# Optimization experiments

Measured on AMD Instinct MI355X. Metric: run time of the kernel, lower is better.

The kernel has to match this reference:

```python
import jax, jax.numpy as jnp
import numpy as np

S = 72
IMG_W, IMG_H = 640, 360
STRIDE = 32
FMAP_H, FMAP_W = IMG_H // STRIDE, IMG_W // STRIDE  # 11, 20
N_OFFSETS = S
N_STRIPS = S - 1
ANGLES = np.array([15.0, 22.0, 30.0, 39.0, 49.0, 60.0, 72.0, 80.0, 90.0, 100.0, 108.0, 120.0, 131.0, 141.0, 150.0, 158.0, 165.0])
N_ANG = 17
N_PRED = 2 + 2 + 1 + N_OFFSETS  # 77
N_EDGE = FMAP_W + 2 * FMAP_H    # 42
N_PROP = N_ANG * N_EDGE         # 714
NMS_THRES = 15.0
BACKBONE_C = 512
CONV_C = 1024


def _make_anchors():
    anchor_ys = np.linspace(1.0, 0.0, N_OFFSETS)
    tan = np.tan(np.deg2rad(ANGLES))
    def side(origins):
        out = np.zeros((N_ANG, N_PRED, len(origins)), np.float32)
        for i, (sx, sy) in enumerate(origins):
            out[:, 2, i] = 1.0 - sy
            out[:, 3, i] = sx
            out[:, 5:, i] = (sx + (sy - anchor_ys)[None, :] / tan[:, None]) * IMG_W
        return out.reshape(N_ANG * N_PRED, len(origins))
    left = side([(0.0, y) for y in np.linspace(1.0, 0.0, FMAP_H)])
    right = side([(1.0, y) for y in np.linspace(1.0, 0.0, FMAP_H)])
    bottom = side([(x, 1.0) for x in np.linspace(1.0, 0.0, FMAP_W)])
    anchors = np.zeros((N_ANG * N_PRED, FMAP_H, FMAP_W), np.float32)
    anchors[:, :, 0] = left
    anchors[:, :, -1] = right
    anchors[:, -1, :] = bottom
    edge = np.concatenate([anchors[:, :, 0], anchors[:, :, -1], anchors[:, -1, :]], 1)  # [1309,42]
    anch_dim = edge.reshape(N_ANG, N_PRED, N_EDGE).transpose(2, 0, 1).reshape(N_PROP, N_PRED)
    return jnp.asarray(anchors), jnp.asarray(anch_dim)


def setup_inputs():
    key = jax.random.key(0)
    ks = jax.random.split(key, 4)
    B = 32
    feat = jax.random.normal(ks[0], (B, BACKBONE_C, FMAP_H, FMAP_W), jnp.float32)
    W_conv = jax.random.normal(ks[1], (CONV_C, BACKBONE_C), jnp.float32) * 0.02
    b_conv = jnp.zeros((CONV_C,), jnp.float32)
    W_cls = jax.random.normal(ks[2], (2 * N_ANG, CONV_C), jnp.float32) * 0.02
    b_cls = jnp.zeros((2 * N_ANG,), jnp.float32)
    W_reg = jax.random.normal(ks[3], (N_ANG * (N_OFFSETS + 1), CONV_C), jnp.float32) * 0.02
    b_reg = jnp.zeros((N_ANG * (N_OFFSETS + 1),), jnp.float32)
    anchors, anchors_anchor_dim = _make_anchors()
    return {"feat": feat, "W_conv": W_conv, "b_conv": b_conv, "W_cls": W_cls, "b_cls": b_cls,
            "W_reg": W_reg, "b_reg": b_reg, "anchors": anchors, "anchors_anchor_dim": anchors_anchor_dim}


def _proposals(feat, W_conv, b_conv, W_cls, b_cls, W_reg, b_reg, anchors):
    B = feat.shape[0]
    features = jnp.einsum('bchw,oc->bohw', feat, W_conv) + b_conv[None, :, None, None]
    cls_f = jnp.einsum('bchw,oc->bohw', features, W_cls) + b_cls[None, :, None, None]
    reg_f = jnp.einsum('bchw,oc->bohw', features, W_reg) + b_reg[None, :, None, None]
    anch = anchors.reshape(N_ANG, N_PRED, FMAP_H, FMAP_W)
    cls_r = cls_f.reshape(B, N_ANG, 2, FMAP_H, FMAP_W)
    reg_r = reg_f.reshape(B, N_ANG, N_OFFSETS + 1, FMAP_H, FMAP_W)
    # slots 0:2 <- cls logits (set), slots 2:4 <- anchor (copied), slots 4: <- anchor + reg
    mid = jnp.broadcast_to(anch[None, :, 2:4], (B, N_ANG, 2, FMAP_H, FMAP_W))
    tail = anch[None, :, 4:] + reg_r
    lane = jnp.concatenate([cls_r, mid, tail], axis=2)  # [B,17,77,h,w]
    # gather the three feature-map edges: left col, right col, bottom row
    edges = jnp.concatenate([lane[:, :, :, :, 0], lane[:, :, :, :, -1], lane[:, :, :, -1, :]], axis=3)  # [B,17,77,42]
    return edges.transpose(0, 3, 1, 2).reshape(B, N_PROP, N_PRED)  # [B,714,77]


def _nms_one(props, scores):
    # greedy line-NMS over proposals of one image, shapes static
    order = jnp.argsort(-scores)
    p = props[order]
    start = jnp.clip(jnp.round(p[:, 2] * N_STRIPS), 0.0, float(N_STRIPS))
    end = jnp.clip(start + p[:, 4] - 1.0, 0.0, float(N_STRIPS))
    xs = p[:, 5:]  # [N,72]
    s = jnp.maximum(start[:, None], start[None, :])
    e = jnp.minimum(end[:, None], end[None, :])
    idx = jnp.arange(N_OFFSETS, dtype=p.dtype)
    m = (idx[None, None, :] >= s[..., None]) & (idx[None, None, :] <= e[..., None])  # [N,N,72]
    diff = jnp.abs(xs[:, None, :] - xs[None, :, :])  # [N,N,72]
    cnt = e - s + 1.0
    dist = jnp.where(cnt > 0, jnp.sum(diff * m, -1) / jnp.maximum(cnt, 1.0), jnp.inf)
    sup = dist < NMS_THRES
    n = p.shape[0]
    pos = jnp.arange(n)
    def step(suppressed, i):
        keep_i = ~suppressed[i]
        suppressed = suppressed | (keep_i & sup[i] & (pos > i))
        return suppressed, keep_i
    _, keep_sorted = jax.lax.scan(step, jnp.zeros(n, bool), pos)
    return jnp.zeros(n, bool).at[order].set(keep_sorted)


def reference(feat, W_conv, b_conv, W_cls, b_cls, W_reg, b_reg, anchors, anchors_anchor_dim):
    proposals = _proposals(feat, W_conv, b_conv, W_cls, b_cls, W_reg, b_reg, anchors)
    scores = jax.nn.softmax(proposals[..., :2], axis=-1)[..., 1]  # [B,714]
    keep_mask = jax.lax.map(lambda pr: _nms_one(pr[0], pr[1]), (proposals, scores))  # [B,714]
    return proposals, keep_mask, scores
```

## Files before the change

### kernel.cpp

```cpp
#include <hip/hip_runtime.h>
#include <math.h>

#define NB     32
#define FH     11
#define FW     20
#define CIN    512
#define CMID   1024
#define NANG   17
#define NPREDD 77
#define NEDGE  42
#define NPROPP 714
#define NOFF   72
#define NCLS   34
#define NREGR  1241
#define N2PAD  1280
#define MTOT   1344
#define NSTRIPSF 71.0f
#define PADK   40

typedef unsigned long long u64;
typedef unsigned short ushortt;
typedef short s8v __attribute__((ext_vector_type(8)));
typedef float f4v __attribute__((ext_vector_type(4)));

__device__ inline ushortt f2bf(float f) {
    unsigned u = __float_as_uint(f);
    u += 0x7fffu + ((u >> 16) & 1u);
    return (ushortt)(u >> 16);
}
__device__ inline float bf2f(ushortt h) {
    return __uint_as_float(((unsigned)h) << 16);
}

__global__ __launch_bounds__(256) void k_gather_split(const float* __restrict__ feat,
                                                      ushortt* __restrict__ Ahi,
                                                      ushortt* __restrict__ Alo)
{
    int idx = blockIdx.x * 256 + threadIdx.x;
    int m = idx >> 9, c = idx & 511;
    int b = m / NEDGE, e = m - b * NEDGE;
    int h, w;
    if (e < FH)          { h = e;      w = 0;      }
    else if (e < 2 * FH) { h = e - FH; w = FW - 1; }
    else                 { h = FH - 1; w = e - 2 * FH; }
    float v = feat[((size_t)(b * CIN + c) * FH + h) * FW + w];
    ushortt hi = f2bf(v);
    Ahi[idx] = hi;
    Alo[idx] = f2bf(v - bf2f(hi));
}

__global__ __launch_bounds__(256) void k_gemm1m(const ushortt* __restrict__ Ahi,
                                                const ushortt* __restrict__ Alo,
                                                const float* __restrict__ W,
                                                const float* __restrict__ bias,
                                                ushortt* __restrict__ Chi,
                                                ushortt* __restrict__ Clo)
{
    const int K = CIN, N = CMID;
    __shared__ __align__(16) ushortt Ash[64 * PADK], Asl[64 * PADK];
    __shared__ __align__(16) ushortt Bsh[64 * PADK], Bsl[64 * PADK];
    int tid = threadIdx.x;
    int m0 = blockIdx.y * 64, n0 = blockIdx.x * 64;
    int srow = tid >> 2, sg = tid & 3;
    int lane = tid & 63, wv = tid >> 6;
    int wm = (wv & 1) * 32, wn = (wv >> 1) * 32;
    int quad = lane >> 4, l15 = lane & 15;

    f4v acc[2][2];
#pragma unroll
    for (int i = 0; i < 2; ++i)
#pragma unroll
        for (int j = 0; j < 2; ++j) acc[i][j] = (f4v){0.f, 0.f, 0.f, 0.f};

    const ushortt* Ahp = Ahi + (size_t)(m0 + srow) * K + sg * 8;
    const ushortt* Alp = Alo + (size_t)(m0 + srow) * K + sg * 8;
    const float*   Wp  = W   + (size_t)(n0 + srow) * K + sg * 8;

    for (int k0 = 0; k0 < K; k0 += 32) {
        __syncthreads();
        s8v av = *(const s8v*)(Ahp + k0);
        s8v lv = *(const s8v*)(Alp + k0);
        float4 w0 = *(const float4*)(Wp + k0);
        float4 w1 = *(const float4*)(Wp + k0 + 4);
        float wf[8] = {w0.x, w0.y, w0.z, w0.w, w1.x, w1.y, w1.z, w1.w};
        s8v wh, wl;
#pragma unroll
        for (int j = 0; j < 8; ++j) {
            ushortt h = f2bf(wf[j]);
            wh[j] = (short)h;
            wl[j] = (short)f2bf(wf[j] - bf2f(h));
        }
        *(s8v*)&Ash[srow * PADK + sg * 8] = av;
        *(s8v*)&Asl[srow * PADK + sg * 8] = lv;
        *(s8v*)&Bsh[srow * PADK + sg * 8] = wh;
        *(s8v*)&Bsl[srow * PADK + sg * 8] = wl;
        __syncthreads();
        s8v ah[2], al[2], bh[2], bl[2];
#pragma unroll
        for (int s = 0; s < 2; ++s) {
            ah[s] = *(const s8v*)&Ash[(wm + s * 16 + l15) * PADK + quad * 8];
            al[s] = *(const s8v*)&Asl[(wm + s * 16 + l15) * PADK + quad * 8];
            bh[s] = *(const s8v*)&Bsh[(wn + s * 16 + l15) * PADK + quad * 8];
            bl[s] = *(const s8v*)&Bsl[(wn + s * 16 + l15) * PADK + quad * 8];
        }
#pragma unroll
        for (int sm = 0; sm < 2; ++sm)
#pragma unroll
            for (int sn = 0; sn < 2; ++sn) {
                acc[sm][sn] = __builtin_amdgcn_mfma_f32_16x16x32_bf16(al[sm], bl[sn], acc[sm][sn], 0, 0, 0);
                acc[sm][sn] = __builtin_amdgcn_mfma_f32_16x16x32_bf16(al[sm], bh[sn], acc[sm][sn], 0, 0, 0);
                acc[sm][sn] = __builtin_amdgcn_mfma_f32_16x16x32_bf16(ah[sm], bl[sn], acc[sm][sn], 0, 0, 0);
                acc[sm][sn] = __builtin_amdgcn_mfma_f32_16x16x32_bf16(ah[sm], bh[sn], acc[sm][sn], 0, 0, 0);
            }
    }
#pragma unroll
    for (int sm = 0; sm < 2; ++sm)
#pragma unroll
        for (int sn = 0; sn < 2; ++sn)
#pragma unroll
            for (int r = 0; r < 4; ++r) {
                int m = m0 + wm + sm * 16 + quad * 4 + r;
                int n = n0 + wn + sn * 16 + l15;
                float v = acc[sm][sn][r] + bias[n];
                ushortt h = f2bf(v);
                Chi[(size_t)m * N + n] = h;
                Clo[(size_t)m * N + n] = f2bf(v - bf2f(h));
            }
}

__global__ __launch_bounds__(256) void k_gemm2m(const ushortt* __restrict__ Ahi,
                                                const ushortt* __restrict__ Alo,
                                                const float* __restrict__ Wcls,
                                                const float* __restrict__ bcls,
                                                const float* __restrict__ Wreg,
                                                const float* __restrict__ breg,
                                                float* __restrict__ C)
{
    const int K = CMID;
    __shared__ __align__(16) ushortt Ash[64 * PADK], Asl[64 * PADK];
    __shared__ __align__(16) ushortt Bsh[64 * PADK], Bsl[64 * PADK];
    int tid = threadIdx.x;
    int m0 = blockIdx.y * 64, n0 = blockIdx.x * 64;
    int srow = tid >> 2, sg = tid & 3;
    int lane = tid & 63, wv = tid >> 6;
    int wm = (wv & 1) * 32, wn = (wv >> 1) * 32;
    int quad = lane >> 4, l15 = lane & 15;

    f4v acc[2][2];
#pragma unroll
    for (int i = 0; i < 2; ++i)
#pragma unroll
        for (int j = 0; j < 2; ++j) acc[i][j] = (f4v){0.f, 0.f, 0.f, 0.f};

    const ushortt* Ahp = Ahi + (size_t)(m0 + srow) * K + sg * 8;
    const ushortt* Alp = Alo + (size_t)(m0 + srow) * K + sg * 8;
    int nrow = n0 + srow;
    const float* Wp = Wcls;
    bool wvalid = true;
    if (nrow < NCLS)              Wp = Wcls + (size_t)nrow * K + sg * 8;
    else if (nrow < NCLS + NREGR) Wp = Wreg + (size_t)(nrow - NCLS) * K + sg * 8;
    else                          wvalid = false;

    for (int k0 = 0; k0 < K; k0 += 32) {
        __syncthreads();
        s8v av = *(const s8v*)(Ahp + k0);
        s8v lv = *(const s8v*)(Alp + k0);
        float4 w0, w1;
        if (wvalid) {
            w0 = *(const float4*)(Wp + k0);
            w1 = *(const float4*)(Wp + k0 + 4);
        } else {
            w0 = make_float4(0.f, 0.f, 0.f, 0.f);
            w1 = w0;
        }
        float wf[8] = {w0.x, w0.y, w0.z, w0.w, w1.x, w1.y, w1.z, w1.w};
        s8v wh, wl;
#pragma unroll
        for (int j = 0; j < 8; ++j) {
            ushortt h = f2bf(wf[j]);
            wh[j] = (short)h;
            wl[j] = (short)f2bf(wf[j] - bf2f(h));
        }
        *(s8v*)&Ash[srow * PADK + sg * 8] = av;
        *(s8v*)&Asl[srow * PADK + sg * 8] = lv;
        *(s8v*)&Bsh[srow * PADK + sg * 8] = wh;
        *(s8v*)&Bsl[srow * PADK + sg * 8] = wl;
        __syncthreads();
        s8v ah[2], al[2], bh[2], bl[2];
#pragma unroll
        for (int s = 0; s < 2; ++s) {
            ah[s] = *(const s8v*)&Ash[(wm + s * 16 + l15) * PADK + quad * 8];
            al[s] = *(const s8v*)&Asl[(wm + s * 16 + l15) * PADK + quad * 8];
            bh[s] = *(const s8v*)&Bsh[(wn + s * 16 + l15) * PADK + quad * 8];
            bl[s] = *(const s8v*)&Bsl[(wn + s * 16 + l15) * PADK + quad * 8];
        }
#pragma unroll
        for (int sm = 0; sm < 2; ++sm)
#pragma unroll
            for (int sn = 0; sn < 2; ++sn) {
                acc[sm][sn] = __builtin_amdgcn_mfma_f32_16x16x32_bf16(al[sm], bl[sn], acc[sm][sn], 0, 0, 0);
                acc[sm][sn] = __builtin_amdgcn_mfma_f32_16x16x32_bf16(al[sm], bh[sn], acc[sm][sn], 0, 0, 0);
                acc[sm][sn] = __builtin_amdgcn_mfma_f32_16x16x32_bf16(ah[sm], bl[sn], acc[sm][sn], 0, 0, 0);
                acc[sm][sn] = __builtin_amdgcn_mfma_f32_16x16x32_bf16(ah[sm], bh[sn], acc[sm][sn], 0, 0, 0);
            }
    }
#pragma unroll
    for (int sm = 0; sm < 2; ++sm)
#pragma unroll
        for (int sn = 0; sn < 2; ++sn)
#pragma unroll
            for (int r = 0; r < 4; ++r) {
                int m = m0 + wm + sm * 16 + quad * 4 + r;
                int n = n0 + wn + sn * 16 + l15;
                float bb = (n < NCLS) ? bcls[n] : ((n < NCLS + NREGR) ? breg[n - NCLS] : 0.f);
                C[(size_t)m * N2PAD + n] = acc[sm][sn][r] + bb;
            }
}

__global__ __launch_bounds__(256) void k_assemble(const float* __restrict__ C2,
                                                  const float* __restrict__ AD,
                                                  float* __restrict__ outP,
                                                  float* __restrict__ outS,
                                                  float* __restrict__ startv,
                                                  float* __restrict__ endv,
                                                  float* __restrict__ xsel)
{
    int mb = blockIdx.x;
    int b = mb / NEDGE, e = mb - b * NEDGE;
    const float* c2 = C2 + (size_t)mb * N2PAD;
    int tid = threadIdx.x;
    for (int idx = tid; idx < NANG * NPREDD; idx += 256) {
        int a = idx / NPREDD, p = idx - a * NPREDD;
        int prop = e * NANG + a;
        float v;
        if (p < 2) v = c2[a * 2 + p];
        else {
            v = AD[prop * NPREDD + p];
            if (p >= 4) v += c2[NCLS + a * 73 + (p - 4)];
        }
        outP[((size_t)b * NPROPP + prop) * NPREDD + p] = v;
    }
    if (tid < NANG) {
        int a = tid, prop = e * NANG + a;
        float c0 = c2[2 * a], c1 = c2[2 * a + 1];
        float mx = fmaxf(c0, c1);
        float e0 = expf(c0 - mx), e1 = expf(c1 - mx);
        outS[b * NPROPP + prop] = e1 / (e0 + e1);
        float p2 = AD[prop * NPREDD + 2];
        float p4 = AD[prop * NPREDD + 4] + c2[NCLS + a * 73];
        float st = fminf(fmaxf(rintf(p2 * NSTRIPSF), 0.0f), NSTRIPSF);
        float en = fminf(fmaxf(st + p4 - 1.0f, 0.0f), NSTRIPSF);
        startv[b * 720 + prop] = st;
        endv[b * 720 + prop] = en;
        int ksi = (int)st;
        xsel[b * 720 + prop] = AD[prop * NPREDD + 5 + ksi] + c2[NCLS + a * 73 + ksi + 1];
    }
}

__global__ __launch_bounds__(128) void k_sort(const float* __restrict__ scores,
                                              int* __restrict__ order)
{
    int b = blockIdx.x, tile = blockIdx.y, tid = threadIdx.x;
    __shared__ __align__(16) float s[720];
    for (int x = tid; x < 720; x += 128)
        s[x] = (x < NPROPP) ? scores[b * NPROPP + x] : -1e30f;
    __syncthreads();
    int i = tile * 128 + tid;
    if (i >= NPROPP) return;
    float si = s[i];
    int r = 0;
#pragma unroll 4
    for (int j4 = 0; j4 < 720; j4 += 4) {
        float4 v = *(const float4*)&s[j4];
        r += (v.x > si) || (v.x == si && (j4 + 0) < i);
        r += (v.y > si) || (v.y == si && (j4 + 1) < i);
        r += (v.z > si) || (v.z == si && (j4 + 2) < i);
        r += (v.w > si) || (v.w == si && (j4 + 3) < i);
    }
    order[b * 720 + r] = i;
}

__global__ __launch_bounds__(256) void k_supmat(const float* __restrict__ outP,
                                                const float* __restrict__ startv,
                                                const float* __restrict__ endv,
                                                const float* __restrict__ xsel,
                                                const int* __restrict__ order,
                                                u64* __restrict__ sup)
{
    int jt = blockIdx.x, it = blockIdx.y, b = blockIdx.z;
    int i0 = it * 64, j0 = jt * 64;
    int tid = threadIdx.x;
    if (j0 + 63 < i0) {
        if (tid < 64) {
            int il = i0 + tid;
            if (il < NPROPP) sup[((size_t)b * NPROPP + il) * 12 + jt] = 0ull;
        }
        return;
    }
    __shared__ float SI[64], EI[64], XI[64];
    __shared__ float SJ[64], EJ[64], XJ[64];
    __shared__ int   OI[64], OJ[64];
    if (tid < 128) {
        int side = tid >> 6, q = tid & 63;
        int pos = (side ? j0 : i0) + q;
        int o = (pos < NPROPP) ? order[b * 720 + pos] : -1;
        float st = (o >= 0) ? startv[b * 720 + o] : 0.f;
        float en = (o >= 0) ? endv[b * 720 + o] : -2.f;
        float xv = (o >= 0) ? xsel[b * 720 + o] : 0.f;
        if (!side) { SI[q] = st; EI[q] = en; XI[q] = xv; OI[q] = o; }
        else       { SJ[q] = st; EJ[q] = en; XJ[q] = xv; OJ[q] = o; }
    }
    __syncthreads();
    int lane = tid & 63, w = tid >> 6;
    int j = j0 + lane;
    float sj = SJ[lane], ej = EJ[lane], xj = XJ[lane];
    const float* basexs = outP + (size_t)b * NPROPP * NPREDD + 5;
#pragma unroll 1
    for (int rep = 0; rep < 16; ++rep) {
        int iloc = w * 16 + rep;
        int il = i0 + iloc;
        float si = SI[iloc], ei = EI[iloc];
        float s = fmaxf(si, sj), e = fminf(ei, ej);
        float cnt = e - s + 1.0f;
        bool sp = false;
        if (cnt > 0.f) {
            if (e < s) {
                sp = true;
            } else {
                int ks = (int)s, ke = (int)e;
                if (si == sj && ke == ks) {
                    sp = (fabsf(XI[iloc] - xj) / fmaxf(cnt, 1.0f)) < 15.0f;
                } else {
                    const float* xi  = basexs + (size_t)OI[iloc] * NPREDD;
                    const float* xjp = basexs + (size_t)OJ[lane] * NPREDD;
                    float sum = 0.f;
                    for (int k = ks; k <= ke; ++k)
                        sum += fabsf(xi[k] - xjp[k]);
                    sp = (sum / fmaxf(cnt, 1.0f)) < 15.0f;
                }
            }
        }
        bool valid = (il < NPROPP) && (j < NPROPP) && (j > il);
        u64 msk = __ballot(valid && sp);
        if (lane == 0 && il < NPROPP)
            sup[((size_t)b * NPROPP + il) * 12 + jt] = msk;
    }
}

__global__ __launch_bounds__(256) void k_scan(const u64* __restrict__ sup,
                                              const int* __restrict__ order,
                                              float* __restrict__ keep_out)
{
    int b = blockIdx.x, tid = threadIdx.x;
    int lane = tid & 63;
    __shared__ u64 K[12], NS[12];
    __shared__ int changed;
    const u64* base = sup + (size_t)b * NPROPP * 12;

    int r0 = tid, r1 = tid + 256, r2 = tid + 512;
    u64 row0[12], row1[12], row2[12];
#pragma unroll
    for (int t = 0; t < 12; ++t) {
        row0[t] = base[(size_t)r0 * 12 + t];
        row1[t] = (r1 < NPROPP) ? base[(size_t)r1 * 12 + t] : 0ull;
        row2[t] = (r2 < NPROPP) ? base[(size_t)r2 * 12 + t] : 0ull;
    }
    if (tid < 12) {
        K[tid] = (tid < 11) ? ~0ull : ((1ull << (NPROPP - 704)) - 1ull);
        NS[tid] = 0ull;
    }
    __syncthreads();

    for (int sweep = 0; sweep < 720; ++sweep) {
        u64 m0 = 0ull - ((K[r0 >> 6] >> (r0 & 63)) & 1ull);
        u64 m1 = (r1 < NPROPP) ? (0ull - ((K[r1 >> 6] >> (r1 & 63)) & 1ull)) : 0ull;
        u64 m2 = (r2 < NPROPP) ? (0ull - ((K[r2 >> 6] >> (r2 & 63)) & 1ull)) : 0ull;
        unsigned lo[12], hi[12];
#pragma unroll
        for (int t = 0; t < 12; ++t) {
            u64 a = (row0[t] & m0) | (row1[t] & m1) | (row2[t] & m2);
            lo[t] = (unsigned)a;
            hi[t] = (unsigned)(a >> 32);
        }
#pragma unroll
        for (int s = 1; s < 64; s <<= 1) {
#pragma unroll
            for (int t = 0; t < 12; ++t) {
                lo[t] |= __shfl_xor(lo[t], s, 64);
                hi[t] |= __shfl_xor(hi[t], s, 64);
            }
        }
        if (tid == 0) changed = 0;
        if (lane == 0) {
#pragma unroll
            for (int t = 0; t < 12; ++t)
                atomicOr(&NS[t], ((u64)hi[t] << 32) | (u64)lo[t]);
        }
        __syncthreads();
        if (tid < 12) {
            u64 valid = (tid < 11) ? ~0ull : ((1ull << (NPROPP - 704)) - 1ull);
            u64 nk = valid & ~NS[tid];
            if (nk != K[tid]) changed = 1;
            K[tid] = nk;
            NS[tid] = 0ull;
        }
        __syncthreads();
        if (!changed) break;
    }
    if (r0 < NPROPP)
        keep_out[b * NPROPP + order[b * 720 + r0]] =
            ((K[r0 >> 6] >> (r0 & 63)) & 1ull) ? 1.f : 0.f;
    if (r1 < NPROPP)
        keep_out[b * NPROPP + order[b * 720 + r1]] =
            ((K[r1 >> 6] >> (r1 & 63)) & 1ull) ? 1.f : 0.f;
    if (r2 < NPROPP)
        keep_out[b * NPROPP + order[b * 720 + r2]] =
            ((K[r2 >> 6] >> (r2 & 63)) & 1ull) ? 1.f : 0.f;
}

extern "C" void kernel_launch(void* const* d_in, const int* in_sizes, int n_in,
                              void* d_out, int out_size, void* d_ws, size_t ws_size,
                              hipStream_t stream)
{
    const float* feat  = (const float*)d_in[0];
    const float* Wconv = (const float*)d_in[1];
    const float* bconv = (const float*)d_in[2];
    const float* Wcls  = (const float*)d_in[3];
    const float* bcls  = (const float*)d_in[4];
    const float* Wreg  = (const float*)d_in[5];
    const float* breg  = (const float*)d_in[6];
    const float* AD    = (const float*)d_in[8];

    float* out  = (float*)d_out;
    float* outP = out;
    float* outK = out + (size_t)NB * NPROPP * NPREDD;
    float* outS = outK + (size_t)NB * NPROPP;

    float* ws = (float*)d_ws;
    ushortt* A1hi = (ushortt*)ws;
    ushortt* A1lo = (ushortt*)(ws + 344064);
    ushortt* A2hi = (ushortt*)(ws + 688128);
    ushortt* A2lo = (ushortt*)(ws + 1376256);
    float*   C2   = ws + 2064384;
    float* startv = ws;
    float* endv   = ws + 23040;
    int*   order  = (int*)(ws + 46080);
    u64*   sup    = (u64*)(ws + 69120);
    float* xsel   = ws + 617472;

    k_gather_split<<<dim3(2688),       dim3(256), 0, stream>>>(feat, A1hi, A1lo);
    k_gemm1m      <<<dim3(16, 21),     dim3(256), 0, stream>>>(A1hi, A1lo, Wconv, bconv, A2hi, A2lo);
    k_gemm2m      <<<dim3(20, 21),     dim3(256), 0, stream>>>(A2hi, A2lo, Wcls, bcls, Wreg, breg, C2);
    k_assemble    <<<dim3(MTOT),       dim3(256), 0, stream>>>(C2, AD, outP, outS, startv, endv, xsel);
    k_sort        <<<dim3(NB, 6),      dim3(128), 0, stream>>>(outS, order);
    k_supmat      <<<dim3(12, 12, NB), dim3(256), 0, stream>>>(outP, startv, endv, xsel, order, sup);
    k_scan        <<<dim3(NB),         dim3(256), 0, stream>>>(sup, order, outK);
}
```

Before: 192.4 us.

## Fuse edge gather into first GEMM and split K across two thread halves

Removes the separate gather/split kernel by having the first GEMM read edge features directly from the feature map and convert them to bf16 hi/lo in registers. Both GEMMs now launch 512 threads per block, with each 256-thread half handling one half of K; partial sums are reduced through shared memory before the epilogue. This targets the low occupancy of the small 336/420-block grids and saves one launch plus a global round trip. The cost is strided, uncoalesced feature loads in the first GEMM and extra shared memory and synchronisation for the reduction.

Result: slower. 197.3 us (+2.5%).

```diff
diff --git a/kernel.cpp b/kernel.cpp
--- a/kernel.cpp
+++ b/kernel.cpp
@@ -32,39 +32,33 @@
     return __uint_as_float(((unsigned)h) << 16);
 }
 
-__global__ __launch_bounds__(256) void k_gather_split(const float* __restrict__ feat,
-                                                      ushortt* __restrict__ Ahi,
-                                                      ushortt* __restrict__ Alo)
-{
-    int idx = blockIdx.x * 256 + threadIdx.x;
-    int m = idx >> 9, c = idx & 511;
-    int b = m / NEDGE, e = m - b * NEDGE;
+__global__ __launch_bounds__(512) void k_gemm1f(const float* __restrict__ feat,
+                                                const float* __restrict__ W,
+                                                const float* __restrict__ bias,
+                                                ushortt* __restrict__ Chi,
+                                                ushortt* __restrict__ Clo)
+{
+    const int K = CIN, K2 = CIN / 2, N = CMID;
+    __shared__ __align__(16) ushortt Ash[2][64 * PADK], Asl[2][64 * PADK];
+    __shared__ __align__(16) ushortt Bsh[2][64 * PADK], Bsl[2][64 * PADK];
+    __shared__ __align__(16) float Pr[64 * 68];
+    int tid = threadIdx.x;
+    int half = tid >> 8, t = tid & 255;
+    int m0 = blockIdx.y * 64, n0 = blockIdx.x * 64;
+    int srow = t >> 2, sg = t & 3;
+    int lane = t & 63, wv = t >> 6;
+    int wm = (wv & 1) * 32, wn = (wv >> 1) * 32;
+    int quad = lane >> 4, l15 = lane & 15;
+
+    int m = m0 + srow;
+    int bb_ = m / NEDGE, e = m - bb_ * NEDGE;
     int h, w;
     if (e < FH)          { h = e;      w = 0;      }
     else if (e < 2 * FH) { h = e - FH; w = FW - 1; }
     else                 { h = FH - 1; w = e - 2 * FH; }
-    float v = feat[((size_t)(b * CIN + c) * FH + h) * FW + w];
-    ushortt hi = f2bf(v);
-    Ahi[idx] = hi;
-    Alo[idx] = f2bf(v - bf2f(hi));
-}
-
-__global__ __launch_bounds__(256) void k_gemm1m(const ushortt* __restrict__ Ahi,
-                                                const ushortt* __restrict__ Alo,
-                                                const float* __restrict__ W,
-                                                const float* __restrict__ bias,
-                                                ushortt* __restrict__ Chi,
-                                                ushortt* __restrict__ Clo)
-{
-    const int K = CIN, N = CMID;
-    __shared__ __align__(16) ushortt Ash[64 * PADK], Asl[64 * PADK];
-    __shared__ __align__(16) ushortt Bsh[64 * PADK], Bsl[64 * PADK];
-    int tid = threadIdx.x;
-    int m0 = blockIdx.y * 64, n0 = blockIdx.x * 64;
-    int srow = tid >> 2, sg = tid & 3;
-    int lane = tid & 63, wv = tid >> 6;
-    int wm = (wv & 1) * 32, wn = (wv >> 1) * 32;
-    int quad = lane >> 4, l15 = lane & 15;
+    const float* fbase = feat + ((size_t)(bb_ * CIN) * FH + h) * FW + w;
+    const int cbase = half * K2 + sg * 8;
+    const float* Wp = W + (size_t)(n0 + srow) * K + half * K2 + sg * 8;
 
     f4v acc[2][2];
 #pragma unroll
@@ -72,36 +66,38 @@
 #pragma unroll
         for (int j = 0; j < 2; ++j) acc[i][j] = (f4v){0.f, 0.f, 0.f, 0.f};
 
-    const ushortt* Ahp = Ahi + (size_t)(m0 + srow) * K + sg * 8;
-    const ushortt* Alp = Alo + (size_t)(m0 + srow) * K + sg * 8;
-    const float*   Wp  = W   + (size_t)(n0 + srow) * K + sg * 8;
-
-    for (int k0 = 0; k0 < K; k0 += 32) {
-        __syncthreads();
-        s8v av = *(const s8v*)(Ahp + k0);
-        s8v lv = *(const s8v*)(Alp + k0);
+    for (int k0 = 0; k0 < K2; k0 += 32) {
+        __syncthreads();
+        s8v ah8, al8;
+#pragma unroll
+        for (int j = 0; j < 8; ++j) {
+            float v = fbase[(size_t)(cbase + k0 + j) * (FH * FW)];
+            ushortt hh_ = f2bf(v);
+            ah8[j] = (short)hh_;
+            al8[j] = (short)f2bf(v - bf2f(hh_));
+        }
         float4 w0 = *(const float4*)(Wp + k0);
         float4 w1 = *(const float4*)(Wp + k0 + 4);
         float wf[8] = {w0.x, w0.y, w0.z, w0.w, w1.x, w1.y, w1.z, w1.w};
         s8v wh, wl;
 #pragma unroll
         for (int j = 0; j < 8; ++j) {
-            ushortt h = f2bf(wf[j]);
-            wh[j] = (short)h;
-            wl[j] = (short)f2bf(wf[j] - bf2f(h));
-        }
-        *(s8v*)&Ash[srow * PADK + sg * 8] = av;
-        *(s8v*)&Asl[srow * PADK + sg * 8] = lv;
-        *(s8v*)&Bsh[srow * PADK + sg * 8] = wh;
-        *(s8v*)&Bsl[srow * PADK + sg * 8] = wl;
+            ushortt hh_ = f2bf(wf[j]);
+            wh[j] = (short)hh_;
+            wl[j] = (short)f2bf(wf[j] - bf2f(hh_));
+        }
+        *(s8v*)&Ash[half][srow * PADK + sg * 8] = ah8;
+        *(s8v*)&Asl[half][srow * PADK + sg * 8] = al8;
+        *(s8v*)&Bsh[half][srow * PADK + sg * 8] = wh;
+        *(s8v*)&Bsl[half][srow * PADK + sg * 8] = wl;
         __syncthreads();
         s8v ah[2], al[2], bh[2], bl[2];
 #pragma unroll
         for (int s = 0; s < 2; ++s) {
-            ah[s] = *(const s8v*)&Ash[(wm + s * 16 + l15) * PADK + quad * 8];
-            al[s] = *(const s8v*)&Asl[(wm + s * 16 + l15) * PADK + quad * 8];
-            bh[s] = *(const s8v*)&Bsh[(wn + s * 16 + l15) * PADK + quad * 8];
-            bl[s] = *(const s8v*)&Bsl[(wn + s * 16 + l15) * PADK + quad * 8];
+            ah[s] = *(const s8v*)&Ash[half][(wm + s * 16 + l15) * PADK + quad * 8];
+            al[s] = *(const s8v*)&Asl[half][(wm + s * 16 + l15) * PADK + quad * 8];
+            bh[s] = *(const s8v*)&Bsh[half][(wn + s * 16 + l15) * PADK + quad * 8];
+            bl[s] = *(const s8v*)&Bsl[half][(wn + s * 16 + l15) * PADK + quad * 8];
         }
 #pragma unroll
         for (int sm = 0; sm < 2; ++sm)
@@ -113,22 +109,35 @@
                 acc[sm][sn] = __builtin_amdgcn_mfma_f32_16x16x32_bf16(ah[sm], bh[sn], acc[sm][sn], 0, 0, 0);
             }
     }
-#pragma unroll
-    for (int sm = 0; sm < 2; ++sm)
-#pragma unroll
-        for (int sn = 0; sn < 2; ++sn)
-#pragma unroll
-            for (int r = 0; r < 4; ++r) {
-                int m = m0 + wm + sm * 16 + quad * 4 + r;
-                int n = n0 + wn + sn * 16 + l15;
-                float v = acc[sm][sn][r] + bias[n];
-                ushortt h = f2bf(v);
-                Chi[(size_t)m * N + n] = h;
-                Clo[(size_t)m * N + n] = f2bf(v - bf2f(h));
-            }
-}
-
-__global__ __launch_bounds__(256) void k_gemm2m(const ushortt* __restrict__ Ahi,
+    __syncthreads();
+    if (half == 1) {
+#pragma unroll
+        for (int sm = 0; sm < 2; ++sm)
+#pragma unroll
+            for (int sn = 0; sn < 2; ++sn)
+#pragma unroll
+                for (int r = 0; r < 4; ++r)
+                    Pr[(wm + sm * 16 + quad * 4 + r) * 68 + wn + sn * 16 + l15] = acc[sm][sn][r];
+    }
+    __syncthreads();
+    if (half == 0) {
+#pragma unroll
+        for (int sm = 0; sm < 2; ++sm)
+#pragma unroll
+            for (int sn = 0; sn < 2; ++sn)
+#pragma unroll
+                for (int r = 0; r < 4; ++r) {
+                    int mm = m0 + wm + sm * 16 + quad * 4 + r;
+                    int n = n0 + wn + sn * 16 + l15;
+                    float v = (acc[sm][sn][r] + Pr[(wm + sm * 16 + quad * 4 + r) * 68 + wn + sn * 16 + l15]) + bias[n];
+                    ushortt hh_ = f2bf(v);
+                    Chi[(size_t)mm * N + n] = hh_;
+                    Clo[(size_t)mm * N + n] = f2bf(v - bf2f(hh_));
+                }
+    }
+}
+
+__global__ __launch_bounds__(512) void k_gemm2f(const ushortt* __restrict__ Ahi,
                                                 const ushortt* __restrict__ Alo,
                                                 const float* __restrict__ Wcls,
                                                 const float* __restrict__ bcls,
@@ -136,32 +145,34 @@
                                                 const float* __restrict__ breg,
                                                 float* __restrict__ C)
 {
-    const int K = CMID;
-    __shared__ __align__(16) ushortt Ash[64 * PADK], Asl[64 * PADK];
-    __shared__ __align__(16) ushortt Bsh[64 * PADK], Bsl[64 * PADK];
+    const int K = CMID, K2 = CMID / 2;
+    __shared__ __align__(16) ushortt Ash[2][64 * PADK], Asl[2][64 * PADK];
+    __shared__ __align__(16) ushortt Bsh[2][64 * PADK], Bsl[2][64 * PADK];
+    __shared__ __align__(16) float Pr[64 * 68];
     int tid = threadIdx.x;
+    int half = tid >> 8, t = tid & 255;
     int m0 = blockIdx.y * 64, n0 = blockIdx.x * 64;
-    int srow = tid >> 2, sg = tid & 3;
-    int lane = tid & 63, wv = tid >> 6;
+    int srow = t >> 2, sg = t & 3;
+    int lane = t & 63, wv = t >> 6;
     int wm = (wv & 1) * 32, wn = (wv >> 1) * 32;
     int quad = lane >> 4, l15 = lane & 15;
 
-    f4v acc[2][2];
-#pragma unroll
-    for (int i = 0; i < 2; ++i)
-#pragma unroll
-        for (int j = 0; j < 2; ++j) acc[i][j] = (f4v){0.f, 0.f, 0.f, 0.f};
-
-    const ushortt* Ahp = Ahi + (size_t)(m0 + srow) * K + sg * 8;
-    const ushortt* Alp = Alo + (size_t)(m0 + srow) * K + sg * 8;
+    const ushortt* Ahp = Ahi + (size_t)(m0 + srow) * K + half * K2 + sg * 8;
+    const ushortt* Alp = Alo + (size_t)(m0 + srow) * K + half * K2 + sg * 8;
     int nrow = n0 + srow;
     const float* Wp = Wcls;
     bool wvalid = true;
-    if (nrow < NCLS)              Wp = Wcls + (size_t)nrow * K + sg * 8;
-    else if (nrow < NCLS + NREGR) Wp = Wreg + (size_t)(nrow - NCLS) * K + sg * 8;
+    if (nrow < NCLS)              Wp = Wcls + (size_t)nrow * K + half * K2 + sg * 8;
+    else if (nrow < NCLS + NREGR) Wp = Wreg + (size_t)(nrow - NCLS) * K + half * K2 + sg * 8;
     else                          wvalid = false;
 
-    for (int k0 = 0; k0 < K; k0 += 32) {
+    f4v acc[2][2];
+#pragma unroll
+    for (int i = 0; i < 2; ++i)
+#pragma unroll
+        for (int j = 0; j < 2; ++j) acc[i][j] = (f4v){0.f, 0.f, 0.f, 0.f};
+
+    for (int k0 = 0; k0 < K2; k0 += 32) {
         __syncthreads();
         s8v av = *(const s8v*)(Ahp + k0);
         s8v lv = *(const s8v*)(Alp + k0);
@@ -177,22 +188,22 @@
         s8v wh, wl;
 #pragma unroll
         for (int j = 0; j < 8; ++j) {
-            ushortt h = f2bf(wf[j]);
-            wh[j] = (short)h;
-            wl[j] = (short)f2bf(wf[j] - bf2f(h));
-        }
-        *(s8v*)&Ash[srow * PADK + sg * 8] = av;
-        *(s8v*)&Asl[srow * PADK + sg * 8] = lv;
-        *(s8v*)&Bsh[srow * PADK + sg * 8] = wh;
-        *(s8v*)&Bsl[srow * PADK + sg * 8] = wl;
+            ushortt hh_ = f2bf(wf[j]);
+            wh[j] = (short)hh_;
+            wl[j] = (short)f2bf(wf[j] - bf2f(hh_));
+        }
+        *(s8v*)&Ash[half][srow * PADK + sg * 8] = av;
+        *(s8v*)&Asl[half][srow * PADK + sg * 8] = lv;
+        *(s8v*)&Bsh[half][srow * PADK + sg * 8] = wh;
+        *(s8v*)&Bsl[half][srow * PADK + sg * 8] = wl;
         __syncthreads();
         s8v ah[2], al[2], bh[2], bl[2];
 #pragma unroll
         for (int s = 0; s < 2; ++s) {
-            ah[s] = *(const s8v*)&Ash[(wm + s * 16 + l15) * PADK + quad * 8];
-            al[s] = *(const s8v*)&Asl[(wm + s * 16 + l15) * PADK + quad * 8];
-            bh[s] = *(const s8v*)&Bsh[(wn + s * 16 + l15) * PADK + quad * 8];
-            bl[s] = *(const s8v*)&Bsl[(wn + s * 16 + l15) * PADK + quad * 8];
+            ah[s] = *(const s8v*)&Ash[half][(wm + s * 16 + l15) * PADK + quad * 8];
+            al[s] = *(const s8v*)&Asl[half][(wm + s * 16 + l15) * PADK + quad * 8];
+            bh[s] = *(const s8v*)&Bsh[half][(wn + s * 16 + l15) * PADK + quad * 8];
+            bl[s] = *(const s8v*)&Bsl[half][(wn + s * 16 + l15) * PADK + quad * 8];
         }
 #pragma unroll
         for (int sm = 0; sm < 2; ++sm)
@@ -204,17 +215,31 @@
                 acc[sm][sn] = __builtin_amdgcn_mfma_f32_16x16x32_bf16(ah[sm], bh[sn], acc[sm][sn], 0, 0, 0);
             }
     }
-#pragma unroll
-    for (int sm = 0; sm < 2; ++sm)
-#pragma unroll
-        for (int sn = 0; sn < 2; ++sn)
-#pragma unroll
-            for (int r = 0; r < 4; ++r) {
-                int m = m0 + wm + sm * 16 + quad * 4 + r;
-                int n = n0 + wn + sn * 16 + l15;
-                float bb = (n < NCLS) ? bcls[n] : ((n < NCLS + NREGR) ? breg[n - NCLS] : 0.f);
-                C[(size_t)m * N2PAD + n] = acc[sm][sn][r] + bb;
-            }
+    __syncthreads();
+    if (half == 1) {
+#pragma unroll
+        for (int sm = 0; sm < 2; ++sm)
+#pragma unroll
+            for (int sn = 0; sn < 2; ++sn)
+#pragma unroll
+                for (int r = 0; r < 4; ++r)
+                    Pr[(wm + sm * 16 + quad * 4 + r) * 68 + wn + sn * 16 + l15] = acc[sm][sn][r];
+    }
+    __syncthreads();
+    if (half == 0) {
+#pragma unroll
+        for (int sm = 0; sm < 2; ++sm)
+#pragma unroll
+            for (int sn = 0; sn < 2; ++sn)
+#pragma unroll
+                for (int r = 0; r < 4; ++r) {
+                    int mm = m0 + wm + sm * 16 + quad * 4 + r;
+                    int n = n0 + wn + sn * 16 + l15;
+                    float bb = (n < NCLS) ? bcls[n] : ((n < NCLS + NREGR) ? breg[n - NCLS] : 0.f);
+                    C[(size_t)mm * N2PAD + n] =
+                        (acc[sm][sn][r] + Pr[(wm + sm * 16 + quad * 4 + r) * 68 + wn + sn * 16 + l15]) + bb;
+                }
+    }
 }
 
 __global__ __launch_bounds__(256) void k_assemble(const float* __restrict__ C2,
@@ -437,8 +462,6 @@
     float* outS = outK + (size_t)NB * NPROPP;
 
     float* ws = (float*)d_ws;
-    ushortt* A1hi = (ushortt*)ws;
-    ushortt* A1lo = (ushortt*)(ws + 344064);
     ushortt* A2hi = (ushortt*)(ws + 688128);
     ushortt* A2lo = (ushortt*)(ws + 1376256);
     float*   C2   = ws + 2064384;
@@ -448,11 +471,10 @@
     u64*   sup    = (u64*)(ws + 69120);
     float* xsel   = ws + 617472;
 
-    k_gather_split<<<dim3(2688),       dim3(256), 0, stream>>>(feat, A1hi, A1lo);
-    k_gemm1m      <<<dim3(16, 21),     dim3(256), 0, stream>>>(A1hi, A1lo, Wconv, bconv, A2hi, A2lo);
-    k_gemm2m      <<<dim3(20, 21),     dim3(256), 0, stream>>>(A2hi, A2lo, Wcls, bcls, Wreg, breg, C2);
-    k_assemble    <<<dim3(MTOT),       dim3(256), 0, stream>>>(C2, AD, outP, outS, startv, endv, xsel);
-    k_sort        <<<dim3(NB, 6),      dim3(128), 0, stream>>>(outS, order);
-    k_supmat      <<<dim3(12, 12, NB), dim3(256), 0, stream>>>(outP, startv, endv, xsel, order, sup);
-    k_scan        <<<dim3(NB),         dim3(256), 0, stream>>>(sup, order, outK);
-}
+    k_gemm1f  <<<dim3(16, 21),     dim3(512), 0, stream>>>(feat, Wconv, bconv, A2hi, A2lo);
+    k_gemm2f  <<<dim3(20, 21),     dim3(512), 0, stream>>>(A2hi, A2lo, Wcls, bcls, Wreg, breg, C2);
+    k_assemble<<<dim3(MTOT),       dim3(256), 0, stream>>>(C2, AD, outP, outS, startv, endv, xsel);
+    k_sort    <<<dim3(NB, 6),      dim3(128), 0, stream>>>(outS, order);
+    k_supmat  <<<dim3(12, 12, NB), dim3(256), 0, stream>>>(outP, startv, endv, xsel, order, sup);
+    k_scan    <<<dim3(NB),         dim3(256), 0, stream>>>(sup, order, outK);
+}
```
